# Performance work log

Hardware: AMD Instinct MI355X
Metric: run time of the kernel (lower is better)

## Reference

```python
import jax, jax.numpy as jnp
from jax import lax
import numpy as np

B, S, D, H = 8, 1024, 512, 8
DH, FF, INNER, K = D // H, 4 * D, 2 * D, 31
SQRT_D = float(np.sqrt(D))  # module scales by sqrt(dim), not sqrt(dim_head)


def _ln(x, g, b, eps=1e-5):
    m = jnp.mean(x, -1, keepdims=True)
    v = jnp.var(x, -1, keepdims=True)
    return (x - m) / jnp.sqrt(v + eps) * g + b


def _swish(x):
    return x * jax.nn.sigmoid(x)


def _ff(x, g, b, w1, b1, w2, b2):
    return _swish(_ln(x, g, b) @ w1 + b1) @ w2 + b2


def _pos_encoding(s, d):
    pos = jnp.arange(s, dtype=jnp.float32)[:, None]
    div = jnp.exp(jnp.arange(0, d, 2, dtype=jnp.float32) * (-np.log(10000.0) / d))
    pe = jnp.zeros((s, d), jnp.float32)
    pe = pe.at[:, 0::2].set(jnp.sin(pos * div))
    pe = pe.at[:, 1::2].set(jnp.cos(pos * div))
    return pe


def _rel_shift(ps):  # (b, h, s, t) Transformer-XL relative shift
    b, h, s, t = ps.shape
    ps = jnp.pad(ps, ((0, 0), (0, 0), (0, 0), (1, 0)))
    return ps.reshape(b, h, t + 1, s)[:, :, 1:].reshape(b, h, s, t)


def _forward(x, ff1_ln_g, ff1_ln_b, ff1_w1, ff1_b1, ff1_w2, ff1_b2,
             attn_ln_g, attn_ln_b, wq, bq, wk, bk, wv, bv, wpos,
             u_bias, v_bias, wo, bo,
             conv_ln_g, conv_ln_b, pw1_w, pw1_b, dw_w, dw_b,
             bn_g, bn_b, bn_mean, bn_var, pw2_w, pw2_b,
             ff2_ln_g, ff2_ln_b, ff2_w1, ff2_b1, ff2_w2, ff2_b2,
             norm_g, norm_b):
    b, s, d = x.shape
    # FF1 half-residual
    x = 0.5 * _ff(x, ff1_ln_g, ff1_ln_b, ff1_w1, ff1_b1, ff1_w2, ff1_b2) + x
    # relative-position multi-head self-attention
    y = _ln(x, attn_ln_g, attn_ln_b)
    q = (y @ wq + bq).reshape(b, s, H, DH)
    k = (y @ wk + bk).reshape(b, s, H, DH)
    v = (y @ wv + bv).reshape(b, s, H, DH)
    pos = (_pos_encoding(s, d) @ wpos).reshape(s, H, DH)  # identical across batch
    score = jnp.einsum('bshd,bthd->bhst', q + u_bias, k)
    pos_score = _rel_shift(jnp.einsum('bshd,thd->bhst', q + v_bias, pos))
    attn = jax.nn.softmax((score + pos_score) / SQRT_D, axis=-1)
    ctx = jnp.einsum('bhst,bthd->bshd', attn, v).reshape(b, s, d)
    x = ctx @ wo + bo + x
    # conformer conv module: LN -> pointwise -> GLU -> depthwise -> BN -> swish -> pointwise
    c = _ln(x, conv_ln_g, conv_ln_b) @ pw1_w + pw1_b  # (b, s, 2*inner)
    a, gate = jnp.split(c, 2, axis=-1)
    z = jnp.transpose(a * jax.nn.sigmoid(gate), (0, 2, 1))  # (b, inner, s)
    z = jnp.pad(z, ((0, 0), (0, 0), (K // 2, K // 2)))  # pad (15, 15) for k=31
    z = lax.conv_general_dilated(z, dw_w[:, None, :], (1,), 'VALID',
                                 dimension_numbers=('NCH', 'OIH', 'NCH'),
                                 feature_group_count=INNER) + dw_b[None, :, None]
    z = (z - bn_mean[None, :, None]) * (bn_g / jnp.sqrt(bn_var + 1e-5))[None, :, None] + bn_b[None, :, None]
    z = _swish(z)
    x = jnp.transpose(z, (0, 2, 1)) @ pw2_w + pw2_b + x
    # FF2 half-residual + final LN
    x = 0.5 * _ff(x, ff2_ln_g, ff2_ln_b, ff2_w1, ff2_b1, ff2_w2, ff2_b2) + x
    return _ln(x, norm_g, norm_b)


def setup_inputs() -> dict:
    key = jax.random.key(0)
    ks = iter(jax.random.split(key, 64))

    def w(shape, scale=0.02):
        return scale * jax.random.normal(next(ks), shape, jnp.float32)

    return {
        'x': jax.random.normal(next(ks), (B, S, D), jnp.float32),
        'ff1_ln_g': jnp.ones(D, jnp.float32), 'ff1_ln_b': jnp.zeros(D, jnp.float32),
        'ff1_w1': w((D, FF)), 'ff1_b1': jnp.zeros(FF, jnp.float32),
        'ff1_w2': w((FF, D)), 'ff1_b2': jnp.zeros(D, jnp.float32),
        'attn_ln_g': jnp.ones(D, jnp.float32), 'attn_ln_b': jnp.zeros(D, jnp.float32),
        'wq': w((D, D)), 'bq': jnp.zeros(D, jnp.float32),
        'wk': w((D, D)), 'bk': jnp.zeros(D, jnp.float32),
        'wv': w((D, D)), 'bv': jnp.zeros(D, jnp.float32),
        'wpos': w((D, D)),
        'u_bias': w((H, DH)), 'v_bias': w((H, DH)),
        'wo': w((D, D)), 'bo': jnp.zeros(D, jnp.float32),
        'conv_ln_g': jnp.ones(D, jnp.float32), 'conv_ln_b': jnp.zeros(D, jnp.float32),
        'pw1_w': w((D, 2 * INNER)), 'pw1_b': jnp.zeros(2 * INNER, jnp.float32),
        'dw_w': w((INNER, K)), 'dw_b': jnp.zeros(INNER, jnp.float32),
        'bn_g': jnp.ones(INNER, jnp.float32), 'bn_b': jnp.zeros(INNER, jnp.float32),
        'bn_mean': jnp.zeros(INNER, jnp.float32), 'bn_var': jnp.ones(INNER, jnp.float32),
        'pw2_w': w((INNER, D)), 'pw2_b': jnp.zeros(D, jnp.float32),
        'ff2_ln_g': jnp.ones(D, jnp.float32), 'ff2_ln_b': jnp.zeros(D, jnp.float32),
        'ff2_w1': w((D, FF)), 'ff2_b1': jnp.zeros(FF, jnp.float32),
        'ff2_w2': w((FF, D)), 'ff2_b2': jnp.zeros(D, jnp.float32),
        'norm_g': jnp.ones(D, jnp.float32), 'norm_b': jnp.zeros(D, jnp.float32),
    }


def reference(x, ff1_ln_g, ff1_ln_b, ff1_w1, ff1_b1, ff1_w2, ff1_b2,
              attn_ln_g, attn_ln_b, wq, bq, wk, bk, wv, bv, wpos,
              u_bias, v_bias, wo, bo,
              conv_ln_g, conv_ln_b, pw1_w, pw1_b, dw_w, dw_b,
              bn_g, bn_b, bn_mean, bn_var, pw2_w, pw2_b,
              ff2_ln_g, ff2_ln_b, ff2_w1, ff2_b1, ff2_w2, ff2_b2,
              norm_g, norm_b):
    return _forward(x, ff1_ln_g, ff1_ln_b, ff1_w1, ff1_b1, ff1_w2, ff1_b2,
                    attn_ln_g, attn_ln_b, wq, bq, wk, bk, wv, bv, wpos,
                    u_bias, v_bias, wo, bo,
                    conv_ln_g, conv_ln_b, pw1_w, pw1_b, dw_w, dw_b,
                    bn_g, bn_b, bn_mean, bn_var, pw2_w, pw2_b,
                    ff2_ln_g, ff2_ln_b, ff2_w1, ff2_b1, ff2_w2, ff2_b2,
                    norm_g, norm_b)
```

## Files before the change

kernel.cpp:

```cpp
#include <hip/hip_runtime.h>
#include <cstdint>
#include <cstddef>

#define B_ 8
#define S_ 1024
#define D_ 512
#define H_ 8
#define DH_ 64
#define FF_ 2048
#define INNER_ 1024
#define NROWS 8192
#define INV_SQRT_D 0.04419417382415922f

typedef __attribute__((ext_vector_type(8))) short bf16x8;
typedef __attribute__((ext_vector_type(4))) float f32x4;
struct alignas(8) short4x { short x, y, z, w; };

__device__ __forceinline__ float sigmoidf_(float x) { return 1.f / (1.f + expf(-x)); }

__device__ __forceinline__ short f2bf(float f) {
  uint32_t u = __float_as_uint(f);
  u += 0x7fff + ((u >> 16) & 1);
  return (short)(u >> 16);
}
__device__ __forceinline__ float bf2f(short s) {
  return __uint_as_float(((uint32_t)(uint16_t)s) << 16);
}

__device__ __forceinline__ void store_out(float* C, size_t i, float v) { C[i] = v; }
__device__ __forceinline__ void store_out(short* C, size_t i, float v) { C[i] = f2bf(v); }

__device__ __forceinline__ void gload_lds16(const void* g, void* lds) {
  __builtin_amdgcn_global_load_lds(
      (const __attribute__((address_space(1))) uint32_t*)g,
      (__attribute__((address_space(3))) uint32_t*)lds, 16, 0, 0);
}

template <typename OutT>
__global__ __launch_bounds__(256) void ln_kernel(const float* __restrict__ in,
    const float* __restrict__ g, const float* __restrict__ b,
    OutT* __restrict__ out) {
  int row = blockIdx.x;
  const float* x = in + (size_t)row * D_;
  OutT* o = out + (size_t)row * D_;
  int t = threadIdx.x;
  float v0 = x[t], v1 = x[t + 256];
  float s = v0 + v1, q = v0 * v0 + v1 * v1;
#pragma unroll
  for (int off = 32; off > 0; off >>= 1) {
    s += __shfl_down(s, off);
    q += __shfl_down(q, off);
  }
  __shared__ float red[8];
  int wid = t >> 6, lane = t & 63;
  if (lane == 0) { red[wid] = s; red[wid + 4] = q; }
  __syncthreads();
  if (t == 0) {
    float S = red[0] + red[1] + red[2] + red[3];
    float Q = red[4] + red[5] + red[6] + red[7];
    float mean = S * (1.f / D_);
    float var = Q * (1.f / D_) - mean * mean;
    red[0] = mean;
    red[1] = rsqrtf(var + 1e-5f);
  }
  __syncthreads();
  float mean = red[0], inv = red[1];
  store_out(o, t, (v0 - mean) * inv * g[t] + b[t]);
  store_out(o, t + 256, (v1 - mean) * inv * g[t + 256] + b[t + 256]);
}

__global__ __launch_bounds__(256) void transpose_bf16_kernel(const float* __restrict__ in,
    short* __restrict__ out, int K, int N) {
  __shared__ float t[32][33];
  int n0 = blockIdx.x << 5, k0 = blockIdx.y << 5;
  int tx = threadIdx.x & 31, ty = threadIdx.x >> 5;
#pragma unroll
  for (int e = 0; e < 4; ++e)
    t[ty + e * 8][tx] = in[(size_t)(k0 + ty + e * 8) * N + n0 + tx];
  __syncthreads();
#pragma unroll
  for (int e = 0; e < 4; ++e)
    out[(size_t)(n0 + ty + e * 8) * K + k0 + tx] = f2bf(t[tx][ty + e * 8]);
}

template <int BN, int EPI, typename OutT>
__global__ __launch_bounds__(256) void mfma_gemm(const short* __restrict__ A,
    const short* __restrict__ Bt, const float* __restrict__ bias,
    const float* __restrict__ res, OutT* __restrict__ C, short* __restrict__ C2,
    const float* __restrict__ bias2, const float* __restrict__ bias3,
    int M, int N, int K) {
  constexpr int NFN = BN / 32;
  constexpr int AL = 4;
  constexpr int BL = BN / 32;
  __shared__ short As[2][128 * 64];
  __shared__ short Bs[2][BN * 64];
  int tid = threadIdx.x;
  int w = tid >> 6, l = tid & 63;
  int nwg = gridDim.x * gridDim.y;
  int flat = blockIdx.y * gridDim.x + blockIdx.x;
  int W = (flat & 7) * (nwg >> 3) + (flat >> 3);
  int bm = (W / gridDim.x) << 7, bn = (W % gridDim.x) * BN;
  int wr = w >> 1, wc = w & 1;
  f32x4 acc[4][NFN] = {};

  const short* a_p[AL];
  int a_d[AL];
#pragma unroll
  for (int e = 0; e < AL; ++e) {
    int fl = e * 256 + w * 64 + l;
    int row = fl >> 3, c = fl & 7;
    int g = c ^ (row & 7);
    a_p[e] = A + (size_t)(bm + row) * K + g * 8;
    a_d[e] = (e * 32 + w * 8) * 64;
  }
  const short* b_p[BL];
  int b_d[BL];
#pragma unroll
  for (int e = 0; e < BL; ++e) {
    int fl = e * 256 + w * 64 + l;
    int row = fl >> 3, c = fl & 7;
    int g = c ^ (row & 7);
    b_p[e] = Bt + (size_t)(bn + row) * K + g * 8;
    b_d[e] = (e * 32 + w * 8) * 64;
  }

  int lcol = l & 15, lk = l >> 4;
  int aoff[4][2], boff[NFN][2];
#pragma unroll
  for (int m = 0; m < 4; ++m) {
    int r = wr * 64 + m * 16 + lcol;
#pragma unroll
    for (int ks = 0; ks < 2; ++ks) {
      int c = ks * 4 + lk;
      aoff[m][ks] = r * 64 + ((c ^ (r & 7)) << 3);
    }
  }
#pragma unroll
  for (int n = 0; n < NFN; ++n) {
    int r = wc * (BN / 2) + n * 16 + lcol;
#pragma unroll
    for (int ks = 0; ks < 2; ++ks) {
      int c = ks * 4 + lk;
      boff[n][ks] = r * 64 + ((c ^ (r & 7)) << 3);
    }
  }

#define STAGE64(kk, bb)                                                        \
  {                                                                            \
    _Pragma("unroll") for (int e = 0; e < AL; ++e)                             \
        gload_lds16(a_p[e] + (kk), &As[bb][a_d[e]]);                           \
    _Pragma("unroll") for (int e = 0; e < BL; ++e)                             \
        gload_lds16(b_p[e] + (kk), &Bs[bb][b_d[e]]);                           \
  }

  int nt = K >> 6;
  STAGE64(0, 0);
  __syncthreads();
  for (int t = 0; t < nt; ++t) {
    int cur = t & 1;
    if (t + 1 < nt) STAGE64((t + 1) << 6, cur ^ 1);
#pragma unroll
    for (int ks = 0; ks < 2; ++ks) {
      bf16x8 af[4], bfr[NFN];
#pragma unroll
      for (int m = 0; m < 4; ++m) af[m] = *(const bf16x8*)(&As[cur][aoff[m][ks]]);
#pragma unroll
      for (int n = 0; n < NFN; ++n) bfr[n] = *(const bf16x8*)(&Bs[cur][boff[n][ks]]);
#pragma unroll
      for (int m = 0; m < 4; ++m)
#pragma unroll
        for (int n = 0; n < NFN; ++n)
          acc[m][n] = __builtin_amdgcn_mfma_f32_16x16x32_bf16(af[m], bfr[n], acc[m][n], 0, 0, 0);
    }
    __syncthreads();
  }
#undef STAGE64

  int lrow = (l >> 4) << 2;
#pragma unroll
  for (int m = 0; m < 4; ++m) {
    int row0 = bm + wr * 64 + m * 16 + lrow;
#pragma unroll
    for (int n = 0; n < NFN; ++n) {
      int col = bn + wc * (BN / 2) + n * 16 + lcol;
      float bv = bias ? bias[col] : 0.f;
      if (EPI == 5) {
        short4x o;
        o.x = f2bf(acc[m][n][0] + bv);
        o.y = f2bf(acc[m][n][1] + bv);
        o.z = f2bf(acc[m][n][2] + bv);
        o.w = f2bf(acc[m][n][3] + bv);
        size_t tidx = ((size_t)(row0 >> 10) * 512 + col) * 1024 + (row0 & 1023);
        *(short4x*)((short*)C + tidx) = o;
      } else if (EPI == 4) {
#pragma unroll
        for (int r = 0; r < 4; ++r) {
          size_t idx = (size_t)(row0 + r) * N + col;
          float v = acc[m][n][r] + bv;
          ((short*)C)[idx] = f2bf(v + bias2[col]);
          C2[idx] = f2bf(v + bias3[col]);
        }
      } else {
#pragma unroll
        for (int r = 0; r < 4; ++r) {
          size_t idx = (size_t)(row0 + r) * N + col;
          float v = acc[m][n][r] + bv;
          if (EPI == 1) v = v * sigmoidf_(v);
          else if (EPI == 2) v = 0.5f * v + res[idx];
          else if (EPI == 3) v = v + res[idx];
          store_out(C, idx, v);
        }
      }
    }
  }
}

__global__ __launch_bounds__(256) void pe_kernel(short* __restrict__ pe) {
  int t = blockIdx.x, i = threadIdx.x;
  float freq = expf((float)(2 * i) * (-9.2103403719761836f / 512.f));
  float arg = (float)t * freq;
  pe[(size_t)t * D_ + 2 * i] = f2bf(sinf(arg));
  pe[(size_t)t * D_ + 2 * i + 1] = f2bf(cosf(arg));
}

__global__ __launch_bounds__(256) void attn_pos_mfma(const short* __restrict__ Qb,
    const short* __restrict__ Pos, short* __restrict__ Out, int bh0) {
  __shared__ short Qs[128 * 64];
  __shared__ short Ks[128 * 64];
  int tid = threadIdx.x;
  int w = tid >> 6, l = tid & 63;
  int z = blockIdx.z;
  int bh = bh0 + z, b = bh >> 3, h = bh & 7;
  int bi = blockIdx.y << 7, bj = blockIdx.x << 7;
  int srow = w * 8 + (l >> 3);
  int sch = l & 7;
#pragma unroll
  for (int cc = 0; cc < 4; ++cc) {
    int r = cc * 32 + srow;
    int g = sch ^ (r & 7);
    gload_lds16(Qb + (size_t)(b * S_ + bi + r) * D_ + h * DH_ + g * 8, Qs + (cc * 32 + w * 8) * 64);
    gload_lds16(Pos + (size_t)(bj + r) * D_ + h * DH_ + g * 8, Ks + (cc * 32 + w * 8) * 64);
  }
  __syncthreads();
  int wr = w >> 1, wc = w & 1;
  int lcol = l & 15, lk = l >> 4;
  bf16x8 qf[4][2], kf[4][2];
#pragma unroll
  for (int m = 0; m < 4; ++m)
#pragma unroll
    for (int ks = 0; ks < 2; ++ks) {
      int r = wr * 64 + m * 16 + lcol;
      int c = ks * 4 + lk;
      qf[m][ks] = *(const bf16x8*)(Qs + r * 64 + ((c ^ (r & 7)) << 3));
    }
#pragma unroll
  for (int n = 0; n < 4; ++n)
#pragma unroll
    for (int ks = 0; ks < 2; ++ks) {
      int r = wc * 64 + n * 16 + lcol;
      int c = ks * 4 + lk;
      kf[n][ks] = *(const bf16x8*)(Ks + r * 64 + ((c ^ (r & 7)) << 3));
    }
  f32x4 acc[4][4] = {};
#pragma unroll
  for (int ks = 0; ks < 2; ++ks)
#pragma unroll
    for (int m = 0; m < 4; ++m)
#pragma unroll
      for (int n = 0; n < 4; ++n)
        acc[m][n] = __builtin_amdgcn_mfma_f32_16x16x32_bf16(qf[m][ks], kf[n][ks], acc[m][n], 0, 0, 0);
  int lrow = (l >> 4) << 2;
  short* Oz = Out + (size_t)z * S_ * S_;
#pragma unroll
  for (int m = 0; m < 4; ++m)
#pragma unroll
    for (int r = 0; r < 4; ++r) {
      int iG = bi + wr * 64 + m * 16 + lrow + r;
#pragma unroll
      for (int n = 0; n < 4; ++n) {
        int tG = bj + wc * 64 + n * 16 + lcol;
        short val = f2bf(acc[m][n][r]);
        if (tG >= S_ - 1 - iG)
          Oz[(size_t)iG * S_ + (tG - (S_ - 1 - iG))] = val;
        else if (iG >= 1)
          Oz[(size_t)(iG - 1) * S_ + (tG + iG + 1)] = val;
        if (tG == 0 && iG < S_ - 1)
          Oz[(size_t)iG * S_ + iG + 1] = 0;
      }
    }
}

__global__ __launch_bounds__(512) void attn_fused(const short* __restrict__ qu,
    const short* __restrict__ kk, const short* __restrict__ vT,
    const short* __restrict__ Psh, short* __restrict__ ctx, int bh0) {
  __shared__ short Ks[2][64 * 64];
  __shared__ short Vs[2][64 * 64];
  __shared__ short Ps[128 * 64];
  int tid = threadIdx.x;
  int w = tid >> 6, l = tid & 63;
  int z = blockIdx.y;
  int bh = bh0 + z, b = bh >> 3, h = bh & 7;
  int i0 = blockIdx.x << 7;
  bf16x8 qf0, qf1;
  {
    const short* qrow = qu + (size_t)(b * S_ + i0 + w * 16 + (l & 15)) * D_ + h * DH_ + ((l >> 4) << 3);
    qf0 = *(const bf16x8*)(qrow);
    qf1 = *(const bf16x8*)(qrow + 32);
  }
  f32x4 po[4] = {};
  float mrow[4], lrw[4];
  int gi[4];
#pragma unroll
  for (int r = 0; r < 4; ++r) {
    mrow[r] = -1e30f;
    lrw[r] = 0.f;
    gi[r] = i0 + w * 16 + ((l >> 4) << 2) + r;
  }
  const short* prow0 = Psh + (size_t)z * S_ * S_ + (size_t)gi[0] * S_ + (l & 15);
  const short* prow1 = prow0 + S_;
  const short* prow2 = prow1 + S_;
  const short* prow3 = prow2 + S_;

  int srw = (w << 3) + (l >> 3);
  int sg = (l & 7) ^ (srw & 7);
  const short* ksrc = kk + (size_t)(b * S_) * D_ + h * DH_ + (sg << 3);
  const short* vsrc = vT + (size_t)(b * 512 + h * DH_ + srw) * 1024 + (sg << 3);
  int sdst = (w << 3) * 64;

#define STAGE_KV(jt, buf)                                                  \
  {                                                                        \
    int j0_ = (jt) << 6;                                                   \
    gload_lds16(ksrc + (size_t)(j0_ + srw) * D_, &Ks[buf][sdst]);          \
    gload_lds16(vsrc + j0_, &Vs[buf][sdst]);                               \
  }

  float pvc[4][4], pvn[4][4];
#define PLOADF(jt, dst)                                                    \
  {                                                                        \
    int j0_ = (jt) << 6;                                                   \
    _Pragma("unroll") for (int n_ = 0; n_ < 4; ++n_) {                     \
      dst[n_][0] = bf2f(prow0[j0_ + (n_ << 4)]);                           \
      dst[n_][1] = bf2f(prow1[j0_ + (n_ << 4)]);                           \
      dst[n_][2] = bf2f(prow2[j0_ + (n_ << 4)]);                           \
      dst[n_][3] = bf2f(prow3[j0_ + (n_ << 4)]);                           \
    }                                                                      \
  }

  STAGE_KV(0, 0);
  PLOADF(0, pvc);
  __syncthreads();

  for (int jt = 0; jt < 16; ++jt) {
    int buf = jt & 1;
    if (jt < 15) {
      STAGE_KV(jt + 1, buf ^ 1);
      PLOADF(jt + 1, pvn);
    }
    f32x4 sc[4] = {};
#pragma unroll
    for (int ks = 0; ks < 2; ++ks)
#pragma unroll
      for (int n = 0; n < 4; ++n) {
        int rj = (n << 4) + (l & 15);
        int ck = (ks << 2) + (l >> 4);
        bf16x8 kf = *(const bf16x8*)(&Ks[buf][rj * 64 + ((ck ^ (rj & 7)) << 3)]);
        sc[n] = __builtin_amdgcn_mfma_f32_16x16x32_bf16(ks == 0 ? qf0 : qf1, kf, sc[n], 0, 0, 0);
      }
    float pm[4];
#pragma unroll
    for (int r = 0; r < 4; ++r) pm[r] = -1e30f;
#pragma unroll
    for (int n = 0; n < 4; ++n)
#pragma unroll
      for (int r = 0; r < 4; ++r) {
        float v = (sc[n][r] + pvc[n][r]) * INV_SQRT_D;
        sc[n][r] = v;
        pm[r] = fmaxf(pm[r], v);
      }
#pragma unroll
    for (int r = 0; r < 4; ++r)
#pragma unroll
      for (int off = 1; off < 16; off <<= 1) pm[r] = fmaxf(pm[r], __shfl_xor(pm[r], off));
    float psum[4];
#pragma unroll
    for (int r = 0; r < 4; ++r) {
      float mn = fmaxf(mrow[r], pm[r]);
      float f = __expf(mrow[r] - mn);
      mrow[r] = mn;
      lrw[r] *= f;
#pragma unroll
      for (int n = 0; n < 4; ++n) po[n][r] *= f;
      psum[r] = 0.f;
    }
#pragma unroll
    for (int n = 0; n < 4; ++n)
#pragma unroll
      for (int r = 0; r < 4; ++r) {
        float p = __expf(sc[n][r] - mrow[r]);
        psum[r] += p;
        int rr = (w << 4) + ((l >> 4) << 2) + r;
        int c = (n << 4) + (l & 15);
        Ps[rr * 64 + (((c >> 3) ^ (rr & 7)) << 3) + (c & 7)] = f2bf(p);
      }
#pragma unroll
    for (int r = 0; r < 4; ++r) {
#pragma unroll
      for (int off = 1; off < 16; off <<= 1) psum[r] += __shfl_xor(psum[r], off);
      lrw[r] += psum[r];
    }
    int rr2 = (w << 4) + (l & 15);
    bf16x8 pa[2];
#pragma unroll
    for (int ks = 0; ks < 2; ++ks) {
      int ck = (ks << 2) + (l >> 4);
      pa[ks] = *(const bf16x8*)(&Ps[rr2 * 64 + ((ck ^ (rr2 & 7)) << 3)]);
    }
#pragma unroll
    for (int ks = 0; ks < 2; ++ks)
#pragma unroll
      for (int n = 0; n < 4; ++n) {
        int rd = (n << 4) + (l & 15);
        int ck = (ks << 2) + (l >> 4);
        bf16x8 vf = *(const bf16x8*)(&Vs[buf][rd * 64 + ((ck ^ (rd & 7)) << 3)]);
        po[n] = __builtin_amdgcn_mfma_f32_16x16x32_bf16(pa[ks], vf, po[n], 0, 0, 0);
      }
    __syncthreads();
    if (jt < 15) {
#pragma unroll
      for (int n = 0; n < 4; ++n)
#pragma unroll
        for (int r = 0; r < 4; ++r) pvc[n][r] = pvn[n][r];
    }
  }
  short* Cz = ctx + (size_t)b * S_ * D_ + h * DH_;
#pragma unroll
  for (int r = 0; r < 4; ++r) {
    float inv = 1.f / lrw[r];
#pragma unroll
    for (int n = 0; n < 4; ++n)
      Cz[(size_t)gi[r] * D_ + (n << 4) + (l & 15)] = f2bf(po[n][r] * inv);
  }
#undef STAGE_KV
#undef PLOADF
}

__global__ __launch_bounds__(256) void glu_kernel(const short* __restrict__ hbuf,
                                                  short* __restrict__ z) {
  size_t idx4 = ((size_t)blockIdx.x * 256 + threadIdx.x) << 2;
  size_t row = idx4 >> 10, c = idx4 & 1023;
  short4x a4 = *(const short4x*)(hbuf + row * 2048 + c);
  short4x g4 = *(const short4x*)(hbuf + row * 2048 + 1024 + c);
  short4x o;
  o.x = f2bf(bf2f(a4.x) * sigmoidf_(bf2f(g4.x)));
  o.y = f2bf(bf2f(a4.y) * sigmoidf_(bf2f(g4.y)));
  o.z = f2bf(bf2f(a4.z) * sigmoidf_(bf2f(g4.z)));
  o.w = f2bf(bf2f(a4.w) * sigmoidf_(bf2f(g4.w)));
  *(short4x*)(z + idx4) = o;
}

#define CTS 32
__global__ __launch_bounds__(256) void dwconv_kernel(const short* __restrict__ z,
    const float* __restrict__ w, const float* __restrict__ wb,
    const float* __restrict__ bng, const float* __restrict__ bnb,
    const float* __restrict__ bnm, const float* __restrict__ bnv,
    short* __restrict__ out) {
  int c = (blockIdx.z << 8) + threadIdx.x;
  int b = blockIdx.y;
  int s0 = blockIdx.x * CTS;
  float wr[31];
#pragma unroll
  for (int kk = 0; kk < 31; ++kk) wr[kk] = w[c * 31 + kk];
  float zv[CTS + 30];
#pragma unroll
  for (int e = 0; e < CTS + 30; ++e) {
    int sr = s0 - 15 + e;
    zv[e] = (sr >= 0 && sr < S_) ? bf2f(z[((size_t)(b * S_ + sr) << 10) + c]) : 0.f;
  }
  float scale = bng[c] * rsqrtf(bnv[c] + 1e-5f);
  float shift = bnb[c] - bnm[c] * scale;
  float bias = wb[c];
#pragma unroll
  for (int s = 0; s < CTS; ++s) {
    float acc = 0.f;
#pragma unroll
    for (int kk = 0; kk < 31; ++kk) acc += zv[s + kk] * wr[kk];
    float v = (acc + bias) * scale + shift;
    v = v * sigmoidf_(v);
    out[((size_t)(b * S_ + s0 + s) << 10) + c] = f2bf(v);
  }
}

extern "C" void kernel_launch(void* const* d_in, const int* in_sizes, int n_in,
                              void* d_out, int out_size, void* d_ws, size_t ws_size,
                              hipStream_t stream) {
  const float* x_in = (const float*)d_in[0];
  const float* ff1_ln_g = (const float*)d_in[1];
  const float* ff1_ln_b = (const float*)d_in[2];
  const float* ff1_w1 = (const float*)d_in[3];
  const float* ff1_b1 = (const float*)d_in[4];
  const float* ff1_w2 = (const float*)d_in[5];
  const float* ff1_b2 = (const float*)d_in[6];
  const float* attn_ln_g = (const float*)d_in[7];
  const float* attn_ln_b = (const float*)d_in[8];
  const float* wq = (const float*)d_in[9];
  const float* bq = (const float*)d_in[10];
  const float* wk = (const float*)d_in[11];
  const float* bk = (const float*)d_in[12];
  const float* wv = (const float*)d_in[13];
  const float* bv = (const float*)d_in[14];
  const float* wpos = (const float*)d_in[15];
  const float* u_bias = (const float*)d_in[16];
  const float* v_bias = (const float*)d_in[17];
  const float* wo = (const float*)d_in[18];
  const float* bo = (const float*)d_in[19];
  const float* conv_ln_g = (const float*)d_in[20];
  const float* conv_ln_b = (const float*)d_in[21];
  const float* pw1_w = (const float*)d_in[22];
  const float* pw1_b = (const float*)d_in[23];
  const float* dw_w = (const float*)d_in[24];
  const float* dw_b = (const float*)d_in[25];
  const float* bn_g = (const float*)d_in[26];
  const float* bn_b = (const float*)d_in[27];
  const float* bn_mean = (const float*)d_in[28];
  const float* bn_var = (const float*)d_in[29];
  const float* pw2_w = (const float*)d_in[30];
  const float* pw2_b = (const float*)d_in[31];
  const float* ff2_ln_g = (const float*)d_in[32];
  const float* ff2_ln_b = (const float*)d_in[33];
  const float* ff2_w1 = (const float*)d_in[34];
  const float* ff2_b1 = (const float*)d_in[35];
  const float* ff2_w2 = (const float*)d_in[36];
  const float* ff2_b2 = (const float*)d_in[37];
  const float* norm_g = (const float*)d_in[38];
  const float* norm_b = (const float*)d_in[39];

  char* wsb = (char*)d_ws;
  float* xb = (float*)(wsb);
  short* yb16 = (short*)(wsb + (16ull << 20));
  short* qu16 = (short*)(wsb + (24ull << 20));
  short* qv16 = (short*)(wsb + (32ull << 20));
  short* k16 = (short*)(wsb + (40ull << 20));
  short* vT16 = (short*)(wsb + (48ull << 20));
  short* ctx16 = (short*)(wsb + (56ull << 20));
  short* pos16 = (short*)(wsb + (64ull << 20));
  short* wt = (short*)(wsb + (65ull << 20));
  short* Pb16 = (short*)(wsb + (80ull << 20));
  short* hb16 = (short*)(wsb + (80ull << 20));
  short* zb16 = (short*)(wsb + (112ull << 20));
  short* cb16 = (short*)(wsb + (128ull << 20));
  short* peb16 = ctx16;

  short* ff1w1t = wt;
  short* ff1w2t = ff1w1t + 2048 * 512;
  short* wqt = ff1w2t + 512 * 2048;
  short* wkt = wqt + 512 * 512;
  short* wvt = wkt + 512 * 512;
  short* wot = wvt + 512 * 512;
  short* wpost = wot + 512 * 512;
  short* pw1t = wpost + 512 * 512;
  short* pw2t = pw1t + 2048 * 512;
  short* ff2w1t = pw2t + 512 * 1024;
  short* ff2w2t = ff2w1t + 2048 * 512;

  dim3 blk(256);

  transpose_bf16_kernel<<<dim3(64, 16), blk, 0, stream>>>(ff1_w1, ff1w1t, 512, 2048);
  transpose_bf16_kernel<<<dim3(16, 64), blk, 0, stream>>>(ff1_w2, ff1w2t, 2048, 512);
  transpose_bf16_kernel<<<dim3(16, 16), blk, 0, stream>>>(wq, wqt, 512, 512);
  transpose_bf16_kernel<<<dim3(16, 16), blk, 0, stream>>>(wk, wkt, 512, 512);
  transpose_bf16_kernel<<<dim3(16, 16), blk, 0, stream>>>(wv, wvt, 512, 512);
  transpose_bf16_kernel<<<dim3(16, 16), blk, 0, stream>>>(wo, wot, 512, 512);
  transpose_bf16_kernel<<<dim3(16, 16), blk, 0, stream>>>(wpos, wpost, 512, 512);
  transpose_bf16_kernel<<<dim3(64, 16), blk, 0, stream>>>(pw1_w, pw1t, 512, 2048);
  transpose_bf16_kernel<<<dim3(16, 32), blk, 0, stream>>>(pw2_w, pw2t, 1024, 512);
  transpose_bf16_kernel<<<dim3(64, 16), blk, 0, stream>>>(ff2_w1, ff2w1t, 512, 2048);
  transpose_bf16_kernel<<<dim3(16, 64), blk, 0, stream>>>(ff2_w2, ff2w2t, 2048, 512);

  ln_kernel<short><<<NROWS, blk, 0, stream>>>(x_in, ff1_ln_g, ff1_ln_b, yb16);
  mfma_gemm<128, 1, short><<<dim3(FF_ / 128, NROWS / 128), blk, 0, stream>>>(yb16, ff1w1t, ff1_b1, nullptr, hb16, nullptr, nullptr, nullptr, NROWS, FF_, D_);
  mfma_gemm<64, 2, float><<<dim3(D_ / 64, NROWS / 128), blk, 0, stream>>>(hb16, ff1w2t, ff1_b2, x_in, xb, nullptr, nullptr, nullptr, NROWS, D_, FF_);

  ln_kernel<short><<<NROWS, blk, 0, stream>>>(xb, attn_ln_g, attn_ln_b, yb16);
  mfma_gemm<64, 4, short><<<dim3(D_ / 64, NROWS / 128), blk, 0, stream>>>(yb16, wqt, bq, nullptr, qu16, qv16, u_bias, v_bias, NROWS, D_, D_);
  mfma_gemm<64, 0, short><<<dim3(D_ / 64, NROWS / 128), blk, 0, stream>>>(yb16, wkt, bk, nullptr, k16, nullptr, nullptr, nullptr, NROWS, D_, D_);
  mfma_gemm<64, 5, short><<<dim3(D_ / 64, NROWS / 128), blk, 0, stream>>>(yb16, wvt, bv, nullptr, vT16, nullptr, nullptr, nullptr, NROWS, D_, D_);
  pe_kernel<<<S_, blk, 0, stream>>>(peb16);
  mfma_gemm<64, 0, short><<<dim3(D_ / 64, S_ / 128), blk, 0, stream>>>(peb16, wpost, nullptr, nullptr, pos16, nullptr, nullptr, nullptr, S_, D_, D_);

  const int CH = 32;
  for (int c = 0; c < 64 / CH; ++c) {
    int bh0 = c * CH;
    attn_pos_mfma<<<dim3(8, 8, CH), blk, 0, stream>>>(qv16, pos16, Pb16, bh0);
    attn_fused<<<dim3(S_ / 128, CH), dim3(512), 0, stream>>>(qu16, k16, vT16, Pb16, ctx16, bh0);
  }
  mfma_gemm<64, 3, float><<<dim3(D_ / 64, NROWS / 128), blk, 0, stream>>>(ctx16, wot, bo, xb, xb, nullptr, nullptr, nullptr, NROWS, D_, D_);

  ln_kernel<short><<<NROWS, blk, 0, stream>>>(xb, conv_ln_g, conv_ln_b, yb16);
  mfma_gemm<128, 0, short><<<dim3(2 * INNER_ / 128, NROWS / 128), blk, 0, stream>>>(yb16, pw1t, pw1_b, nullptr, hb16, nullptr, nullptr, nullptr, NROWS, 2 * INNER_, D_);
  glu_kernel<<<NROWS * INNER_ / 1024, blk, 0, stream>>>(hb16, zb16);
  dwconv_kernel<<<dim3(S_ / CTS, B_, 4), blk, 0, stream>>>(zb16, dw_w, dw_b, bn_g, bn_b, bn_mean, bn_var, cb16);
  mfma_gemm<64, 3, float><<<dim3(D_ / 64, NROWS / 128), blk, 0, stream>>>(cb16, pw2t, pw2_b, xb, xb, nullptr, nullptr, nullptr, NROWS, D_, INNER_);

  ln_kernel<short><<<NROWS, blk, 0, stream>>>(xb, ff2_ln_g, ff2_ln_b, yb16);
  mfma_gemm<128, 1, short><<<dim3(FF_ / 128, NROWS / 128), blk, 0, stream>>>(yb16, ff2w1t, ff2_b1, nullptr, hb16, nullptr, nullptr, nullptr, NROWS, FF_, D_);
  mfma_gemm<64, 2, float><<<dim3(D_ / 64, NROWS / 128), blk, 0, stream>>>(hb16, ff2w2t, ff2_b2, xb, xb, nullptr, nullptr, nullptr, NROWS, D_, FF_);

  ln_kernel<float><<<NROWS, blk, 0, stream>>>(xb, norm_g, norm_b, (float*)d_out);
}
```

Baseline: 487.3 us.

## Fuse QKV projections, fuse pointwise conv with GLU, vectorize layernorm

Merges the three Q/K/V projection GEMMs into one GEMM with N=1536. Its new epilogue routes each column group to the u/v-biased Q outputs, K, or the transposed V layout. Adds a dedicated pw1 GEMM that computes the value and gate halves together and applies GLU in registers, which removes the separate GLU kernel and the round trip through the full 2048-wide intermediate buffer. Layernorm now uses float2 loads and paired stores, and the FF first GEMMs switch from 128- to 64-wide N tiles. The fused QKV path assumes the transposed wq/wk/wv weight buffers sit back to back in memory.

Result: faster. 464.0 us (median of 2 runs) (-4.8%).

```diff
diff --git a/kernel.cpp b/kernel.cpp
--- a/kernel.cpp
+++ b/kernel.cpp
@@ -15,6 +15,7 @@
 typedef __attribute__((ext_vector_type(8))) short bf16x8;
 typedef __attribute__((ext_vector_type(4))) float f32x4;
 struct alignas(8) short4x { short x, y, z, w; };
+struct alignas(4) short2x { short x, y; };
 
 __device__ __forceinline__ float sigmoidf_(float x) { return 1.f / (1.f + expf(-x)); }
 
@@ -29,6 +30,13 @@
 
 __device__ __forceinline__ void store_out(float* C, size_t i, float v) { C[i] = v; }
 __device__ __forceinline__ void store_out(short* C, size_t i, float v) { C[i] = f2bf(v); }
+__device__ __forceinline__ void store2(float* o, size_t i, float a, float b) {
+  *(float2*)(o + i) = make_float2(a, b);
+}
+__device__ __forceinline__ void store2(short* o, size_t i, float a, float b) {
+  short2x t{f2bf(a), f2bf(b)};
+  *(short2x*)(o + i) = t;
+}
 
 __device__ __forceinline__ void gload_lds16(const void* g, void* lds) {
   __builtin_amdgcn_global_load_lds(
@@ -41,11 +49,10 @@
     const float* __restrict__ g, const float* __restrict__ b,
     OutT* __restrict__ out) {
   int row = blockIdx.x;
-  const float* x = in + (size_t)row * D_;
-  OutT* o = out + (size_t)row * D_;
+  const float2* x2 = (const float2*)(in + (size_t)row * D_);
   int t = threadIdx.x;
-  float v0 = x[t], v1 = x[t + 256];
-  float s = v0 + v1, q = v0 * v0 + v1 * v1;
+  float2 p = x2[t];
+  float s = p.x + p.y, q = p.x * p.x + p.y * p.y;
 #pragma unroll
   for (int off = 32; off > 0; off >>= 1) {
     s += __shfl_down(s, off);
@@ -65,8 +72,11 @@
   }
   __syncthreads();
   float mean = red[0], inv = red[1];
-  store_out(o, t, (v0 - mean) * inv * g[t] + b[t]);
-  store_out(o, t + 256, (v1 - mean) * inv * g[t + 256] + b[t + 256]);
+  float2 gg = ((const float2*)g)[t];
+  float2 bb = ((const float2*)b)[t];
+  store2(out, (size_t)row * D_ + 2 * t,
+         (p.x - mean) * inv * gg.x + bb.x,
+         (p.y - mean) * inv * gg.y + bb.y);
 }
 
 __global__ __launch_bounds__(256) void transpose_bf16_kernel(const float* __restrict__ in,
@@ -88,6 +98,8 @@
     const short* __restrict__ Bt, const float* __restrict__ bias,
     const float* __restrict__ res, OutT* __restrict__ C, short* __restrict__ C2,
     const float* __restrict__ bias2, const float* __restrict__ bias3,
+    const float* __restrict__ bias4, const float* __restrict__ bias5,
+    short* __restrict__ C3, short* __restrict__ C4,
     int M, int N, int K) {
   constexpr int NFN = BN / 32;
   constexpr int AL = 4;
@@ -183,33 +195,151 @@
 #pragma unroll
     for (int n = 0; n < NFN; ++n) {
       int col = bn + wc * (BN / 2) + n * 16 + lcol;
-      float bv = bias ? bias[col] : 0.f;
-      if (EPI == 5) {
-        short4x o;
-        o.x = f2bf(acc[m][n][0] + bv);
-        o.y = f2bf(acc[m][n][1] + bv);
-        o.z = f2bf(acc[m][n][2] + bv);
-        o.w = f2bf(acc[m][n][3] + bv);
-        size_t tidx = ((size_t)(row0 >> 10) * 512 + col) * 1024 + (row0 & 1023);
-        *(short4x*)((short*)C + tidx) = o;
-      } else if (EPI == 4) {
-#pragma unroll
-        for (int r = 0; r < 4; ++r) {
-          size_t idx = (size_t)(row0 + r) * N + col;
-          float v = acc[m][n][r] + bv;
-          ((short*)C)[idx] = f2bf(v + bias2[col]);
-          C2[idx] = f2bf(v + bias3[col]);
+      if (EPI == 7) {
+        int grp = col >> 9;
+        if (grp == 0) {
+          float bv = bias[col];
+          float ub = bias2[col];
+          float vb2 = bias3[col];
+#pragma unroll
+          for (int r = 0; r < 4; ++r) {
+            size_t idx = (size_t)(row0 + r) * 512 + col;
+            float v = acc[m][n][r] + bv;
+            ((short*)C)[idx] = f2bf(v + ub);
+            C2[idx] = f2bf(v + vb2);
+          }
+        } else if (grp == 1) {
+          int c = col - 512;
+          float bv = bias4[c];
+#pragma unroll
+          for (int r = 0; r < 4; ++r)
+            C3[(size_t)(row0 + r) * 512 + c] = f2bf(acc[m][n][r] + bv);
+        } else {
+          int c = col - 1024;
+          float bv = bias5[c];
+          short4x o;
+          o.x = f2bf(acc[m][n][0] + bv);
+          o.y = f2bf(acc[m][n][1] + bv);
+          o.z = f2bf(acc[m][n][2] + bv);
+          o.w = f2bf(acc[m][n][3] + bv);
+          size_t tidx = ((size_t)(row0 >> 10) * 512 + c) * 1024 + (row0 & 1023);
+          *(short4x*)(C4 + tidx) = o;
         }
       } else {
-#pragma unroll
-        for (int r = 0; r < 4; ++r) {
-          size_t idx = (size_t)(row0 + r) * N + col;
-          float v = acc[m][n][r] + bv;
-          if (EPI == 1) v = v * sigmoidf_(v);
-          else if (EPI == 2) v = 0.5f * v + res[idx];
-          else if (EPI == 3) v = v + res[idx];
-          store_out(C, idx, v);
+        float bv = bias ? bias[col] : 0.f;
+        if (EPI == 5) {
+          short4x o;
+          o.x = f2bf(acc[m][n][0] + bv);
+          o.y = f2bf(acc[m][n][1] + bv);
+          o.z = f2bf(acc[m][n][2] + bv);
+          o.w = f2bf(acc[m][n][3] + bv);
+          size_t tidx = ((size_t)(row0 >> 10) * 512 + col) * 1024 + (row0 & 1023);
+          *(short4x*)((short*)C + tidx) = o;
+        } else {
+#pragma unroll
+          for (int r = 0; r < 4; ++r) {
+            size_t idx = (size_t)(row0 + r) * N + col;
+            float v = acc[m][n][r] + bv;
+            if (EPI == 1) v = v * sigmoidf_(v);
+            else if (EPI == 2) v = 0.5f * v + res[idx];
+            else if (EPI == 3) v = v + res[idx];
+            store_out(C, idx, v);
+          }
         }
+      }
+    }
+  }
+}
+
+__global__ __launch_bounds__(256) void pw1_glu_gemm(const short* __restrict__ A,
+    const short* __restrict__ Bt, const float* __restrict__ bias,
+    short* __restrict__ Z) {
+  __shared__ short As[2][128 * 32];
+  __shared__ short Bs[2][128 * 32];
+  int tid = threadIdx.x;
+  int w = tid >> 6, l = tid & 63;
+  int nwg = gridDim.x * gridDim.y;
+  int flat = blockIdx.y * gridDim.x + blockIdx.x;
+  int W = (flat & 7) * (nwg >> 3) + (flat >> 3);
+  int bm = (W / gridDim.x) << 7;
+  int bn = (W % gridDim.x) << 6;
+  int wr = w >> 1, wc = w & 1;
+  f32x4 accA[4][2] = {}, accG[4][2] = {};
+
+  int sr = l >> 2, sc = l & 3;
+  int ra0 = (w * 2 + 0) * 16 + sr;
+  int ra1 = (w * 2 + 1) * 16 + sr;
+  int ga0 = sc ^ ((ra0 >> 1) & 3);
+  int ga1 = sc ^ ((ra1 >> 1) & 3);
+  const short* a0 = A + (size_t)(bm + ra0) * 512 + ga0 * 8;
+  const short* a1 = A + (size_t)(bm + ra1) * 512 + ga1 * 8;
+  int rb0 = (ra0 < 64) ? (bn + ra0) : (1024 + bn + ra0 - 64);
+  int rb1 = (ra1 < 64) ? (bn + ra1) : (1024 + bn + ra1 - 64);
+  const short* b0 = Bt + (size_t)rb0 * 512 + ga0 * 8;
+  const short* b1 = Bt + (size_t)rb1 * 512 + ga1 * 8;
+  int asd0 = (w * 2 + 0) * 512;
+  int asd1 = (w * 2 + 1) * 512;
+
+  int lcol = l & 15, lk = l >> 4;
+  int aoff[4], boff[2][2];
+#pragma unroll
+  for (int m = 0; m < 4; ++m) {
+    int r = wr * 64 + m * 16 + lcol;
+    aoff[m] = r * 32 + ((lk ^ ((r >> 1) & 3)) << 3);
+  }
+#pragma unroll
+  for (int p = 0; p < 2; ++p)
+#pragma unroll
+    for (int n = 0; n < 2; ++n) {
+      int r = p * 64 + wc * 32 + n * 16 + lcol;
+      boff[p][n] = r * 32 + ((lk ^ ((r >> 1) & 3)) << 3);
+    }
+
+#define STAGE32(kk, bb)                            \
+  {                                                \
+    gload_lds16(a0 + (kk), &As[bb][asd0]);         \
+    gload_lds16(a1 + (kk), &As[bb][asd1]);         \
+    gload_lds16(b0 + (kk), &Bs[bb][asd0]);         \
+    gload_lds16(b1 + (kk), &Bs[bb][asd1]);         \
+  }
+
+  STAGE32(0, 0);
+  __syncthreads();
+  for (int t = 0; t < 16; ++t) {
+    int cur = t & 1;
+    if (t + 1 < 16) STAGE32((t + 1) << 5, cur ^ 1);
+    bf16x8 af[4], bA[2], bG[2];
+#pragma unroll
+    for (int m = 0; m < 4; ++m) af[m] = *(const bf16x8*)(&As[cur][aoff[m]]);
+#pragma unroll
+    for (int n = 0; n < 2; ++n) {
+      bA[n] = *(const bf16x8*)(&Bs[cur][boff[0][n]]);
+      bG[n] = *(const bf16x8*)(&Bs[cur][boff[1][n]]);
+    }
+#pragma unroll
+    for (int m = 0; m < 4; ++m)
+#pragma unroll
+      for (int n = 0; n < 2; ++n) {
+        accA[m][n] = __builtin_amdgcn_mfma_f32_16x16x32_bf16(af[m], bA[n], accA[m][n], 0, 0, 0);
+        accG[m][n] = __builtin_amdgcn_mfma_f32_16x16x32_bf16(af[m], bG[n], accG[m][n], 0, 0, 0);
+      }
+    __syncthreads();
+  }
+#undef STAGE32
+
+  int lrow = (l >> 4) << 2;
+#pragma unroll
+  for (int m = 0; m < 4; ++m) {
+    int row0 = bm + wr * 64 + m * 16 + lrow;
+#pragma unroll
+    for (int n = 0; n < 2; ++n) {
+      int col = bn + wc * 32 + n * 16 + lcol;
+      float ba = bias[col], bg = bias[1024 + col];
+#pragma unroll
+      for (int r = 0; r < 4; ++r) {
+        float a = accA[m][n][r] + ba;
+        float g = accG[m][n][r] + bg;
+        Z[(size_t)(row0 + r) * 1024 + col] = f2bf(a * sigmoidf_(g));
       }
     }
   }
@@ -442,20 +572,6 @@
   }
 #undef STAGE_KV
 #undef PLOADF
-}
-
-__global__ __launch_bounds__(256) void glu_kernel(const short* __restrict__ hbuf,
-                                                  short* __restrict__ z) {
-  size_t idx4 = ((size_t)blockIdx.x * 256 + threadIdx.x) << 2;
-  size_t row = idx4 >> 10, c = idx4 & 1023;
-  short4x a4 = *(const short4x*)(hbuf + row * 2048 + c);
-  short4x g4 = *(const short4x*)(hbuf + row * 2048 + 1024 + c);
-  short4x o;
-  o.x = f2bf(bf2f(a4.x) * sigmoidf_(bf2f(g4.x)));
-  o.y = f2bf(bf2f(a4.y) * sigmoidf_(bf2f(g4.y)));
-  o.z = f2bf(bf2f(a4.z) * sigmoidf_(bf2f(g4.z)));
-  o.w = f2bf(bf2f(a4.w) * sigmoidf_(bf2f(g4.w)));
-  *(short4x*)(z + idx4) = o;
 }
 
 #define CTS 32
@@ -576,16 +692,22 @@
   transpose_bf16_kernel<<<dim3(64, 16), blk, 0, stream>>>(ff2_w1, ff2w1t, 512, 2048);
   transpose_bf16_kernel<<<dim3(16, 64), blk, 0, stream>>>(ff2_w2, ff2w2t, 2048, 512);
 
+#define GEMM_ARGS(Abuf, Bbuf, biasp, resp, Cp) \
+  Abuf, Bbuf, biasp, resp, Cp, nullptr, nullptr, nullptr, nullptr, nullptr, nullptr, nullptr
+
   ln_kernel<short><<<NROWS, blk, 0, stream>>>(x_in, ff1_ln_g, ff1_ln_b, yb16);
-  mfma_gemm<128, 1, short><<<dim3(FF_ / 128, NROWS / 128), blk, 0, stream>>>(yb16, ff1w1t, ff1_b1, nullptr, hb16, nullptr, nullptr, nullptr, NROWS, FF_, D_);
-  mfma_gemm<64, 2, float><<<dim3(D_ / 64, NROWS / 128), blk, 0, stream>>>(hb16, ff1w2t, ff1_b2, x_in, xb, nullptr, nullptr, nullptr, NROWS, D_, FF_);
+  mfma_gemm<64, 1, short><<<dim3(FF_ / 64, NROWS / 128), blk, 0, stream>>>(
+      GEMM_ARGS(yb16, ff1w1t, ff1_b1, nullptr, hb16), NROWS, FF_, D_);
+  mfma_gemm<64, 2, float><<<dim3(D_ / 64, NROWS / 128), blk, 0, stream>>>(
+      GEMM_ARGS(hb16, ff1w2t, ff1_b2, x_in, xb), NROWS, D_, FF_);
 
   ln_kernel<short><<<NROWS, blk, 0, stream>>>(xb, attn_ln_g, attn_ln_b, yb16);
-  mfma_gemm<64, 4, short><<<dim3(D_ / 64, NROWS / 128), blk, 0, stream>>>(yb16, wqt, bq, nullptr, qu16, qv16, u_bias, v_bias, NROWS, D_, D_);
-  mfma_gemm<64, 0, short><<<dim3(D_ / 64, NROWS / 128), blk, 0, stream>>>(yb16, wkt, bk, nullptr, k16, nullptr, nullptr, nullptr, NROWS, D_, D_);
-  mfma_gemm<64, 5, short><<<dim3(D_ / 64, NROWS / 128), blk, 0, stream>>>(yb16, wvt, bv, nullptr, vT16, nullptr, nullptr, nullptr, NROWS, D_, D_);
+  mfma_gemm<64, 7, short><<<dim3(1536 / 64, NROWS / 128), blk, 0, stream>>>(
+      yb16, wqt, bq, nullptr, qu16, qv16, u_bias, v_bias, bk, bv, k16, vT16,
+      NROWS, 1536, D_);
   pe_kernel<<<S_, blk, 0, stream>>>(peb16);
-  mfma_gemm<64, 0, short><<<dim3(D_ / 64, S_ / 128), blk, 0, stream>>>(peb16, wpost, nullptr, nullptr, pos16, nullptr, nullptr, nullptr, S_, D_, D_);
+  mfma_gemm<64, 0, short><<<dim3(D_ / 64, S_ / 128), blk, 0, stream>>>(
+      GEMM_ARGS(peb16, wpost, nullptr, nullptr, pos16), S_, D_, D_);
 
   const int CH = 32;
   for (int c = 0; c < 64 / CH; ++c) {
@@ -593,17 +715,21 @@
     attn_pos_mfma<<<dim3(8, 8, CH), blk, 0, stream>>>(qv16, pos16, Pb16, bh0);
     attn_fused<<<dim3(S_ / 128, CH), dim3(512), 0, stream>>>(qu16, k16, vT16, Pb16, ctx16, bh0);
   }
-  mfma_gemm<64, 3, float><<<dim3(D_ / 64, NROWS / 128), blk, 0, stream>>>(ctx16, wot, bo, xb, xb, nullptr, nullptr, nullptr, NROWS, D_, D_);
+  mfma_gemm<64, 3, float><<<dim3(D_ / 64, NROWS / 128), blk, 0, stream>>>(
+      GEMM_ARGS(ctx16, wot, bo, xb, xb), NROWS, D_, D_);
 
   ln_kernel<short><<<NROWS, blk, 0, stream>>>(xb, conv_ln_g, conv_ln_b, yb16);
-  mfma_gemm<128, 0, short><<<dim3(2 * INNER_ / 128, NROWS / 128), blk, 0, stream>>>(yb16, pw1t, pw1_b, nullptr, hb16, nullptr, nullptr, nullptr, NROWS, 2 * INNER_, D_);
-  glu_kernel<<<NROWS * INNER_ / 1024, blk, 0, stream>>>(hb16, zb16);
+  pw1_glu_gemm<<<dim3(INNER_ / 64, NROWS / 128), blk, 0, stream>>>(yb16, pw1t, pw1_b, zb16);
   dwconv_kernel<<<dim3(S_ / CTS, B_, 4), blk, 0, stream>>>(zb16, dw_w, dw_b, bn_g, bn_b, bn_mean, bn_var, cb16);
-  mfma_gemm<64, 3, float><<<dim3(D_ / 64, NROWS / 128), blk, 0, stream>>>(cb16, pw2t, pw2_b, xb, xb, nullptr, nullptr, nullptr, NROWS, D_, INNER_);
+  mfma_gemm<64, 3, float><<<dim3(D_ / 64, NROWS / 128), blk, 0, stream>>>(
+      GEMM_ARGS(cb16, pw2t, pw2_b, xb, xb), NROWS, D_, INNER_);
 
   ln_kernel<short><<<NROWS, blk, 0, stream>>>(xb, ff2_ln_g, ff2_ln_b, yb16);
-  mfma_gemm<128, 1, short><<<dim3(FF_ / 128, NROWS / 128), blk, 0, stream>>>(yb16, ff2w1t, ff2_b1, nullptr, hb16, nullptr, nullptr, nullptr, NROWS, FF_, D_);
-  mfma_gemm<64, 2, float><<<dim3(D_ / 64, NROWS / 128), blk, 0, stream>>>(hb16, ff2w2t, ff2_b2, xb, xb, nullptr, nullptr, nullptr, NROWS, D_, FF_);
+  mfma_gemm<64, 1, short><<<dim3(FF_ / 64, NROWS / 128), blk, 0, stream>>>(
+      GEMM_ARGS(yb16, ff2w1t, ff2_b1, nullptr, hb16), NROWS, FF_, D_);
+  mfma_gemm<64, 2, float><<<dim3(D_ / 64, NROWS / 128), blk, 0, stream>>>(
+      GEMM_ARGS(hb16, ff2w2t, ff2_b2, xb, xb), NROWS, D_, FF_);
 
   ln_kernel<float><<<NROWS, blk, 0, stream>>>(xb, norm_g, norm_b, (float*)d_out);
-}
+#undef GEMM_ARGS
+}
```
